# Kernel tuning notes

Measured on AMD Instinct MI355X. Metric: run time of the kernel, lower is better.

Reference implementation:

```python
import jax, jax.numpy as jnp
import numpy as np

N_MBED = 384
HEAD_SIZE = 64

def setup_inputs() -> dict:
    key = jax.random.key(0)
    kx, kq, kk, kv = jax.random.split(key, 4)
    B, T = 128, 256
    x = jax.random.normal(kx, (B, T, N_MBED), dtype=jnp.float32)
    # torch nn.Linear(n_mbed, head_size, bias=False): y = x @ W^T, W:[head_size, n_mbed].
    # We store the transposed weight [n_mbed, head_size] so y = x @ W.
    s = 1.0 / np.sqrt(N_MBED)
    Wq = jax.random.uniform(kq, (N_MBED, HEAD_SIZE), jnp.float32, -s, s)
    Wk = jax.random.uniform(kk, (N_MBED, HEAD_SIZE), jnp.float32, -s, s)
    Wv = jax.random.uniform(kv, (N_MBED, HEAD_SIZE), jnp.float32, -s, s)
    return {"x": x, "Wq": Wq, "Wk": Wk, "Wv": Wv}

def reference(x, Wq, Wk, Wv):
    B, T, C = x.shape  # C = n_mbed = 384
    q = x @ Wq  # [B,T,H]
    k = x @ Wk
    v = x @ Wv
    # Faithful to source: wei = k @ q^T, scaled by C**-0.5 (C = n_mbed, not head_size)
    wei = jnp.einsum('bth,bsh->bts', k, q) * (C ** -0.5)  # [B,T,T]
    mask = jnp.tril(jnp.ones((T, T), dtype=bool))
    wei = jnp.where(mask, wei, -jnp.inf)
    wei = jax.nn.softmax(wei, axis=-1)
    # dropout omitted (eval mode / identity)
    out = jnp.einsum('bts,bsh->bth', wei, v)  # [B,T,H]
    return out
```

## Files before the change

### kernel.cpp

```cpp
#include <hip/hip_runtime.h>
#include <hip/hip_bf16.h>
#include <math.h>

constexpr int kB = 128;
constexpr int kT = 256;
constexpr int kC = 384;
constexpr int kH = 64;

using bf16x8 = __attribute__((ext_vector_type(8))) short;
using f32x4  = __attribute__((ext_vector_type(4))) float;

union BF4 { short4 s; __hip_bfloat162 h[2]; };

__device__ inline short4 cvt4(float4 a) {
    BF4 u;
    u.h[0] = __float22bfloat162_rn(float2{a.x, a.y});
    u.h[1] = __float22bfloat162_rn(float2{a.z, a.w});
    return u.s;
}
__device__ inline short bf1(float f) {
    __hip_bfloat16 h = __float2bfloat16(f);
    return *(short*)&h;
}

__global__ void prep_kernel(const float* __restrict__ Wq,
                            const float* __restrict__ Wk,
                            const float* __restrict__ Wv,
                            __hip_bfloat16* __restrict__ Wt) {
    int idx = blockIdx.x * 256 + threadIdx.x;
    int n = idx / kC, c = idx % kC;
    int w = n >> 6, h = n & 63;
    const float* W = (w == 0) ? Wq : (w == 1) ? Wk : Wv;
    float val = W[c * kH + h];
    if (w == 1) val *= 0.07362222374744683f;
    Wt[idx] = __float2bfloat16(val);
}

__global__ __launch_bounds__(512, 2) void fused_kernel(
    const float* __restrict__ x, const __hip_bfloat16* __restrict__ Wt,
    float* __restrict__ out)
{
    __shared__ short Qs[256 * 72];
    __shared__ short Ks[128 * 72];
    __shared__ short VTs[64 * 264];
    __shared__ short As[2][256 * 36];
    __shared__ short Bs[2][192 * 36];

    const int bid  = blockIdx.x;
    const int b    = ((bid >> 4) << 3) | (bid & 7);
    const int half = ((bid >> 3) & 1) ^ 1;
    const int t0   = half * 128;

    const int tid  = threadIdx.x;
    const int wave = tid >> 6, lane = tid & 63;
    const int m16  = lane & 15, quad = lane >> 4;
    const int wm = wave & 1, wn = wave >> 1;
    const short* wt = (const short*)Wt;
    const float* xb = x + (size_t)b * kT * kC;

    const bool mfmaAct = (half == 1) || (wm == 0);

    bool kskip[3];
#pragma unroll
    for (int j = 0; j < 3; ++j) {
        const int nt = wn * 3 + j;
        kskip[j] = (half == 1) && (wm == 0) && (nt >= 4) && (nt < 8);
    }

    const int arow = tid >> 1, acol = (tid & 1) * 16;
    const bool aAct = (half == 1) || (arow < 128);

    float4 la[4]; bf16x8 lb0, lb1;
    auto glod = [&](int k0) {
        if (aAct) {
#pragma unroll
            for (int i = 0; i < 4; ++i)
                la[i] = *(const float4*)(xb + (size_t)arow * kC + k0 + acol + 4 * i);
        }
        {
            int n = tid >> 2, kk = (tid & 3) * 8;
            lb0 = *(const bf16x8*)(wt + (size_t)n * kC + k0 + kk);
        }
        if (tid < 256) {
            int c = tid + 512;
            int n = c >> 2, kk = (c & 3) * 8;
            lb1 = *(const bf16x8*)(wt + (size_t)n * kC + k0 + kk);
        }
    };
    auto swr = [&](int d) {
        if (aAct) {
#pragma unroll
            for (int i = 0; i < 4; ++i)
                *(short4*)&As[d][arow * 36 + acol + 4 * i] = cvt4(la[i]);
        }
        {
            int n = tid >> 2, kk = (tid & 3) * 8;
            *(bf16x8*)&Bs[d][n * 36 + kk] = lb0;
        }
        if (tid < 256) {
            int c = tid + 512;
            int n = c >> 2, kk = (c & 3) * 8;
            *(bf16x8*)&Bs[d][n * 36 + kk] = lb1;
        }
    };

    f32x4 acc[8][3];
#pragma unroll
    for (int mt = 0; mt < 8; ++mt)
#pragma unroll
        for (int j = 0; j < 3; ++j) acc[mt][j] = f32x4{0.f, 0.f, 0.f, 0.f};

    glod(0);
    swr(0);
    __syncthreads();

    for (int s = 0; s < 12; ++s) {
        const int d = s & 1;
        if (s < 11) glod((s + 1) * 32);

        if (mfmaAct) {
            bf16x8 af[8];
#pragma unroll
            for (int mt = 0; mt < 8; ++mt)
                af[mt] = *(const bf16x8*)&As[d][(wm * 128 + mt * 16 + m16) * 36 + quad * 8];
#pragma unroll
            for (int j = 0; j < 3; ++j) {
                if (!kskip[j]) {
                    const bf16x8 bfr =
                        *(const bf16x8*)&Bs[d][((wn * 3 + j) * 16 + m16) * 36 + quad * 8];
#pragma unroll
                    for (int mt = 0; mt < 8; ++mt)
                        acc[mt][j] = __builtin_amdgcn_mfma_f32_16x16x32_bf16(
                            af[mt], bfr, acc[mt][j], 0, 0, 0);
                }
            }
        }

        if (s < 11) {
            swr(d ^ 1);
            __syncthreads();
        }
    }

    if (mfmaAct) {
#pragma unroll
        for (int mt = 0; mt < 8; ++mt) {
            const int mbase = wm * 128 + mt * 16 + quad * 4;
#pragma unroll
            for (int j = 0; j < 3; ++j) {
                const int nt = wn * 3 + j;
                const int w  = nt >> 2;
                const int h  = (nt & 3) * 16 + m16;
                if (w == 2) {
                    float4 f = make_float4(acc[mt][j][0], acc[mt][j][1],
                                           acc[mt][j][2], acc[mt][j][3]);
                    *(short4*)&VTs[h * 264 + mbase] = cvt4(f);
                } else if (w == 1) {
                    if ((mbase >> 7) == half) {
#pragma unroll
                        for (int r = 0; r < 4; ++r)
                            Ks[(mbase + r - t0) * 72 + h] = bf1(acc[mt][j][r]);
                    }
                } else {
#pragma unroll
                    for (int r = 0; r < 4; ++r)
                        Qs[(mbase + r) * 72 + h] = bf1(acc[mt][j][r]);
                }
            }
        }
    }
    __syncthreads();

    const int wband = t0 + wave * 16;
    short* Pb = &As[0][0] + wave * 1152;

    const bf16x8 ka0 = *(const bf16x8*)&Ks[(wave * 16 + m16) * 72 + quad * 8];
    const bf16x8 ka1 = *(const bf16x8*)&Ks[(wave * 16 + m16) * 72 + quad * 8 + 32];

    const int ilast = wband >> 6;
    const int jmaxd = wave & 3;

    f32x4 S[4][4];
    const f32x4 Z = f32x4{0.f, 0.f, 0.f, 0.f};
#pragma unroll
    for (int i = 0; i < 4; ++i)
#pragma unroll
        for (int j = 0; j < 4; ++j) S[i][j] = Z;

    __builtin_amdgcn_s_setprio(1);
#pragma unroll
    for (int i = 0; i < 4; ++i) {
        if (i <= ilast) {
#pragma unroll
            for (int j = 0; j < 4; ++j) {
                if (i < ilast || j <= jmaxd) {
                    const int s = i * 64 + j * 16 + m16;
                    bf16x8 qb0 = *(const bf16x8*)&Qs[s * 72 + quad * 8];
                    bf16x8 qb1 = *(const bf16x8*)&Qs[s * 72 + quad * 8 + 32];
                    S[i][j] = __builtin_amdgcn_mfma_f32_16x16x32_bf16(qb0, ka0, S[i][j], 0, 0, 0);
                    S[i][j] = __builtin_amdgcn_mfma_f32_16x16x32_bf16(qb1, ka1, S[i][j], 0, 0, 0);
                }
            }
        }
    }
    __builtin_amdgcn_s_setprio(0);

#pragma unroll
    for (int i = 0; i < 4; ++i)
#pragma unroll
        for (int j = 0; j < 4; ++j)
            if (i == ilast && j == jmaxd) {
#pragma unroll
                for (int r = 0; r < 4; ++r)
                    if (quad * 4 + r > m16) S[i][j][r] = -INFINITY;
            }

    float rm = -INFINITY;
#pragma unroll
    for (int i = 0; i < 4; ++i)
#pragma unroll
        for (int j = 0; j < 4; ++j)
            if (i <= ilast && (i < ilast || j <= jmaxd))
#pragma unroll
                for (int r = 0; r < 4; ++r) rm = fmaxf(rm, S[i][j][r]);
    rm = fmaxf(rm, __shfl_xor(rm, 16, 64));
    rm = fmaxf(rm, __shfl_xor(rm, 32, 64));

    float l_ = 0.f;
#pragma unroll
    for (int i = 0; i < 4; ++i)
#pragma unroll
        for (int j = 0; j < 4; ++j)
            if (i <= ilast && (i < ilast || j <= jmaxd))
#pragma unroll
                for (int r = 0; r < 4; ++r) {
                    const float e = exp2f(S[i][j][r] - rm);
                    S[i][j][r] = e;
                    l_ += e;
                }
    l_ += __shfl_xor(l_, 16, 64);
    l_ += __shfl_xor(l_, 32, 64);

    f32x4 O[4];
#pragma unroll
    for (int i = 0; i < 4; ++i) O[i] = f32x4{0.f, 0.f, 0.f, 0.f};

#pragma unroll
    for (int i = 0; i < 4; ++i) {
        if (i <= ilast) {
            bf16x8 vb[4][2];
#pragma unroll
            for (int ht = 0; ht < 4; ++ht) {
                vb[ht][0] = *(const bf16x8*)&VTs[(ht * 16 + m16) * 264 + i * 64 + quad * 8];
                vb[ht][1] = *(const bf16x8*)&VTs[(ht * 16 + m16) * 264 + i * 64 + quad * 8 + 32];
            }
#pragma unroll
            for (int j = 0; j < 4; ++j)
#pragma unroll
                for (int p = 0; p < 2; ++p) {
                    __hip_bfloat162 w = __float22bfloat162_rn(
                        float2{S[i][j][2 * p], S[i][j][2 * p + 1]});
                    *(__hip_bfloat162*)&Pb[m16 * 72 + j * 16 + quad * 4 + 2 * p] = w;
                }
            bf16x8 pf0 = *(const bf16x8*)&Pb[m16 * 72 + quad * 8];
            bf16x8 pf1 = *(const bf16x8*)&Pb[m16 * 72 + quad * 8 + 32];

            __builtin_amdgcn_s_setprio(1);
#pragma unroll
            for (int ht = 0; ht < 4; ++ht) {
                O[ht] = __builtin_amdgcn_mfma_f32_16x16x32_bf16(pf0, vb[ht][0], O[ht], 0, 0, 0);
                O[ht] = __builtin_amdgcn_mfma_f32_16x16x32_bf16(pf1, vb[ht][1], O[ht], 0, 0, 0);
            }
            __builtin_amdgcn_s_setprio(0);
        }
    }

    float lbc[4];
#pragma unroll
    for (int r = 0; r < 4; ++r)
        lbc[r] = __shfl(l_, (quad << 4) | (quad * 4 + r), 64);
#pragma unroll
    for (int r = 0; r < 4; ++r) {
        const float inv = 1.f / lbc[r];
        const size_t row = (size_t)(b * kT + wband + quad * 4 + r);
#pragma unroll
        for (int ht = 0; ht < 4; ++ht)
            out[row * kH + ht * 16 + m16] = O[ht][r] * inv;
    }
}

extern "C" void kernel_launch(void* const* d_in, const int* in_sizes, int n_in,
                              void* d_out, int out_size, void* d_ws, size_t ws_size,
                              hipStream_t stream) {
    const float* x  = (const float*)d_in[0];
    const float* Wq = (const float*)d_in[1];
    const float* Wk = (const float*)d_in[2];
    const float* Wv = (const float*)d_in[3];
    float* out = (float*)d_out;

    __hip_bfloat16* Wt = (__hip_bfloat16*)d_ws;

    prep_kernel<<<(192 * kC) / 256, 256, 0, stream>>>(Wq, Wk, Wv, Wt);
    fused_kernel<<<dim3(256), 512, 0, stream>>>(x, Wt, out);
}
```

Measured before the change: 110.6 us.

## Interleave 16-row query bands across block pair to balance causal work

Previously each batch was split into two blocks by contiguous halves of T, so the first-half block had much less causal attention work and skipped part of the projection. Now each block takes interleaved 16-row bands (even or odd), computing Q/V projections for all rows and K only for its own bands. This balances attention work between the two blocks of a batch, so neither waits on a heavier partner. The cost is that both blocks now do full x loads and Q/V projection MFMAs, where the lower-half block used to skip roughly half of them.

```diff
diff --git a/kernel.cpp b/kernel.cpp
--- a/kernel.cpp
+++ b/kernel.cpp
@@ -48,8 +48,7 @@
 
     const int bid  = blockIdx.x;
     const int b    = ((bid >> 4) << 3) | (bid & 7);
-    const int half = ((bid >> 3) & 1) ^ 1;
-    const int t0   = half * 128;
+    const int blk  = (bid >> 3) & 1;
 
     const int tid  = threadIdx.x;
     const int wave = tid >> 6, lane = tid & 63;
@@ -58,25 +57,13 @@
     const short* wt = (const short*)Wt;
     const float* xb = x + (size_t)b * kT * kC;
 
-    const bool mfmaAct = (half == 1) || (wm == 0);
-
-    bool kskip[3];
-#pragma unroll
-    for (int j = 0; j < 3; ++j) {
-        const int nt = wn * 3 + j;
-        kskip[j] = (half == 1) && (wm == 0) && (nt >= 4) && (nt < 8);
-    }
-
     const int arow = tid >> 1, acol = (tid & 1) * 16;
-    const bool aAct = (half == 1) || (arow < 128);
 
     float4 la[4]; bf16x8 lb0, lb1;
     auto glod = [&](int k0) {
-        if (aAct) {
-#pragma unroll
-            for (int i = 0; i < 4; ++i)
-                la[i] = *(const float4*)(xb + (size_t)arow * kC + k0 + acol + 4 * i);
-        }
+#pragma unroll
+        for (int i = 0; i < 4; ++i)
+            la[i] = *(const float4*)(xb + (size_t)arow * kC + k0 + acol + 4 * i);
         {
             int n = tid >> 2, kk = (tid & 3) * 8;
             lb0 = *(const bf16x8*)(wt + (size_t)n * kC + k0 + kk);
@@ -88,11 +75,9 @@
         }
     };
     auto swr = [&](int d) {
-        if (aAct) {
-#pragma unroll
-            for (int i = 0; i < 4; ++i)
-                *(short4*)&As[d][arow * 36 + acol + 4 * i] = cvt4(la[i]);
-        }
+#pragma unroll
+        for (int i = 0; i < 4; ++i)
+            *(short4*)&As[d][arow * 36 + acol + 4 * i] = cvt4(la[i]);
         {
             int n = tid >> 2, kk = (tid & 3) * 8;
             *(bf16x8*)&Bs[d][n * 36 + kk] = lb0;
@@ -104,6 +89,13 @@
         }
     };
 
+    bool isK[3];
+#pragma unroll
+    for (int j = 0; j < 3; ++j) {
+        const int nt = wn * 3 + j;
+        isK[j] = (nt >= 4) && (nt < 8);
+    }
+
     f32x4 acc[8][3];
 #pragma unroll
     for (int mt = 0; mt < 8; ++mt)
@@ -118,18 +110,18 @@
         const int d = s & 1;
         if (s < 11) glod((s + 1) * 32);
 
-        if (mfmaAct) {
+        {
             bf16x8 af[8];
 #pragma unroll
             for (int mt = 0; mt < 8; ++mt)
                 af[mt] = *(const bf16x8*)&As[d][(wm * 128 + mt * 16 + m16) * 36 + quad * 8];
 #pragma unroll
             for (int j = 0; j < 3; ++j) {
-                if (!kskip[j]) {
-                    const bf16x8 bfr =
-                        *(const bf16x8*)&Bs[d][((wn * 3 + j) * 16 + m16) * 36 + quad * 8];
-#pragma unroll
-                    for (int mt = 0; mt < 8; ++mt)
+                const bf16x8 bfr =
+                    *(const bf16x8*)&Bs[d][((wn * 3 + j) * 16 + m16) * 36 + quad * 8];
+#pragma unroll
+                for (int mt = 0; mt < 8; ++mt) {
+                    if (!isK[j] || ((mt & 1) == blk))
                         acc[mt][j] = __builtin_amdgcn_mfma_f32_16x16x32_bf16(
                             af[mt], bfr, acc[mt][j], 0, 0, 0);
                 }
@@ -142,43 +134,43 @@
         }
     }
 
-    if (mfmaAct) {
-#pragma unroll
-        for (int mt = 0; mt < 8; ++mt) {
-            const int mbase = wm * 128 + mt * 16 + quad * 4;
-#pragma unroll
-            for (int j = 0; j < 3; ++j) {
-                const int nt = wn * 3 + j;
-                const int w  = nt >> 2;
-                const int h  = (nt & 3) * 16 + m16;
-                if (w == 2) {
-                    float4 f = make_float4(acc[mt][j][0], acc[mt][j][1],
-                                           acc[mt][j][2], acc[mt][j][3]);
-                    *(short4*)&VTs[h * 264 + mbase] = cvt4(f);
-                } else if (w == 1) {
-                    if ((mbase >> 7) == half) {
-#pragma unroll
-                        for (int r = 0; r < 4; ++r)
-                            Ks[(mbase + r - t0) * 72 + h] = bf1(acc[mt][j][r]);
-                    }
-                } else {
+#pragma unroll
+    for (int mt = 0; mt < 8; ++mt) {
+        const int mbase = wm * 128 + mt * 16 + quad * 4;
+#pragma unroll
+        for (int j = 0; j < 3; ++j) {
+            const int nt = wn * 3 + j;
+            const int w  = nt >> 2;
+            const int h  = (nt & 3) * 16 + m16;
+            if (w == 2) {
+                float4 f = make_float4(acc[mt][j][0], acc[mt][j][1],
+                                       acc[mt][j][2], acc[mt][j][3]);
+                *(short4*)&VTs[h * 264 + mbase] = cvt4(f);
+            } else if (w == 1) {
+                if ((mt & 1) == blk) {
+                    const int slot = wm * 4 + (mt >> 1);
 #pragma unroll
                     for (int r = 0; r < 4; ++r)
-                        Qs[(mbase + r) * 72 + h] = bf1(acc[mt][j][r]);
-                }
+                        Ks[(slot * 16 + quad * 4 + r) * 72 + h] = bf1(acc[mt][j][r]);
+                }
+            } else {
+#pragma unroll
+                for (int r = 0; r < 4; ++r)
+                    Qs[(mbase + r) * 72 + h] = bf1(acc[mt][j][r]);
             }
         }
     }
     __syncthreads();
 
-    const int wband = t0 + wave * 16;
+    const int band  = 2 * wave + blk;
+    const int wband = band * 16;
     short* Pb = &As[0][0] + wave * 1152;
 
     const bf16x8 ka0 = *(const bf16x8*)&Ks[(wave * 16 + m16) * 72 + quad * 8];
     const bf16x8 ka1 = *(const bf16x8*)&Ks[(wave * 16 + m16) * 72 + quad * 8 + 32];
 
-    const int ilast = wband >> 6;
-    const int jmaxd = wave & 3;
+    const int ilast = band >> 2;
+    const int jmaxd = band & 3;
 
     f32x4 S[4][4];
     const f32x4 Z = f32x4{0.f, 0.f, 0.f, 0.f};
```

New measurement: 106.4 us. -3.8%, faster.
